# Kernel tuning notes

Measured on AMD Instinct MI355X. Metric: run time of the kernel, lower is better.

## Reference

```python
import jax, jax.numpy as jnp
import numpy as np

M, B, U, Z, H, X = 16, 2048, 16, 64, 512, 3072


def setup_inputs() -> dict:
    key = jax.random.key(0)
    ks = jax.random.split(key, 9)
    sc = lambda d: 1.0 / np.sqrt(d)
    return {
        "s": jax.random.normal(ks[0], (M, B, U + Z), dtype=jnp.float32),
        # per-mixture z2z: Linear(Z, Z); weights stored as [in, out]
        "Wzz": jax.random.normal(ks[1], (M, Z, Z), dtype=jnp.float32) * sc(Z),
        "bzz": jax.random.normal(ks[2], (M, Z), dtype=jnp.float32) * sc(Z),
        # per-mixture z2h: Linear(Z, H)
        "Wzh": jax.random.normal(ks[3], (M, Z, H), dtype=jnp.float32) * sc(Z),
        "bzh": jax.random.normal(ks[4], (M, H), dtype=jnp.float32) * sc(Z),
        # shared h2hd: Linear(H, H)
        "Whd": jax.random.normal(ks[5], (H, H), dtype=jnp.float32) * sc(H),
        "bhd": jax.random.normal(ks[6], (H,), dtype=jnp.float32) * sc(H),
        "Whx": jax.random.normal(ks[7], (H, X), dtype=jnp.float32) * sc(H),
        "bhx": jax.random.normal(ks[8], (X,), dtype=jnp.float32) * sc(H),
    }


def reference(s, Wzz, bzz, Wzh, bzh, Whd, bhd, Whx, bhx):
    # s: [M, B, U+Z]; split off z (u is unused in non-tvae mode)
    z = s[..., U:U + Z]                                   # [M, B, Z]
    # per-mixture z2z then z2h (batched over mixture dim), fused relu
    zz = jnp.einsum("mbz,mzy->mby", z, Wzz) + bzz[:, None, :]   # [M, B, Z]
    h = jax.nn.relu(jnp.einsum("mbz,mzh->mbh", zz, Wzh) + bzh[:, None, :])  # [M, B, H]
    # shared h2hd (num_layers == 1, h_dim_dec is None)
    h = jax.nn.relu(h @ Whd + bhd)                        # [M, B, H]
    xx = jax.nn.sigmoid(h @ Whx + bhx)                    # [M, B, X]
    return xx
```

## Files before the change

kernel.cpp:

```cpp
#include <hip/hip_runtime.h>
#include <stdint.h>

typedef __attribute__((ext_vector_type(4))) float f32x4;
typedef __attribute__((ext_vector_type(8))) short short8;

#define MM 16
#define BB 2048
#define UU 16
#define ZD 64
#define HH 512
#define XD 3072
#define RTOT (MM * BB)

#define MFMA16(a, b, c) __builtin_amdgcn_mfma_f32_16x16x32_bf16(a, b, c, 0, 0, 0)

static __device__ __forceinline__ unsigned short f2bf(float f) {
  union { float f; uint32_t u; } v; v.f = f;
  uint32_t r = v.u + 0x7fffu + ((v.u >> 16) & 1u);
  return (unsigned short)(r >> 16);
}

static __device__ __forceinline__ void async16(const void* g, void* l) {
  __builtin_amdgcn_global_load_lds(
      (const __attribute__((address_space(1))) uint32_t*)g,
      (__attribute__((address_space(3))) uint32_t*)l, 16, 0, 0);
}

static __device__ __forceinline__ void tr_tile(const float* __restrict__ in,
                                               unsigned short* __restrict__ out,
                                               int R, int C, int c0, int r0, int z,
                                               float (*tile)[33]) {
  const size_t base = (size_t)z * R * C;
  const int tx = threadIdx.x & 31, ty = threadIdx.x >> 5;
#pragma unroll
  for (int k = 0; k < 32; k += 8)
    tile[ty + k][tx] = in[base + (size_t)(r0 + ty + k) * C + c0 + tx];
  __syncthreads();
#pragma unroll
  for (int k = 0; k < 32; k += 8)
    out[base + (size_t)(c0 + ty + k) * R + r0 + tx] = f2bf(tile[tx][ty + k]);
}

__global__ __launch_bounds__(256) void trconv_all(
    const float* __restrict__ Wzz, const float* __restrict__ Wzh,
    const float* __restrict__ Whd, const float* __restrict__ Whx,
    unsigned short* __restrict__ wzzT, unsigned short* __restrict__ wzhT,
    unsigned short* __restrict__ whdT, unsigned short* __restrict__ whxT) {
  __shared__ float tile[32][33];
  int b = blockIdx.x;
  if (b < 64) {
    int l = b;
    tr_tile(Wzz, wzzT, 64, 64, (l & 1) * 32, ((l >> 1) & 1) * 32, l >> 2, tile);
  } else if (b < 576) {
    int l = b - 64;
    tr_tile(Wzh, wzhT, 64, 512, (l & 15) * 32, ((l >> 4) & 1) * 32, l >> 5, tile);
  } else if (b < 832) {
    int l = b - 576;
    tr_tile(Whd, whdT, 512, 512, (l & 15) * 32, (l >> 4) * 32, 0, tile);
  } else {
    int l = b - 832;
    tr_tile(Whx, whxT, 512, 3072, (l % 96) * 32, (l / 96) * 32, 0, tile);
  }
}

__global__ __launch_bounds__(256) void stage12(
    const float* __restrict__ s, const unsigned short* __restrict__ wzzT,
    const unsigned short* __restrict__ wzhT, const float* __restrict__ bzz,
    const float* __restrict__ bzh, unsigned short* __restrict__ h1) {
  __shared__ __align__(16) unsigned short zA[128 * 64];
  __shared__ __align__(16) unsigned short wzz[64 * 64];
  __shared__ __align__(16) unsigned short wbuf[2][128 * 64];
  const int m = blockIdx.y;
  const int m0r = blockIdx.x * 128;
  const int t = threadIdx.x, lane = t & 63, w = t >> 6;
  const int l15 = lane & 15, l4 = lane >> 4;

  {
    const unsigned short* g = wzzT + (size_t)m * 64 * 64;
    async16(g + t * 8, &wzz[t * 8]);
    async16(g + (t + 256) * 8, &wzz[(t + 256) * 8]);
    const unsigned short* gh = wzhT + (size_t)m * 512 * 64;
#pragma unroll
    for (int it = 0; it < 4; ++it) {
      int id = it * 256 + t;
      async16(gh + id * 8, &wbuf[0][id * 8]);
    }
  }
  const float* sb = s + ((size_t)m * BB + m0r) * (UU + ZD) + UU;
#pragma unroll
  for (int it = 0; it < 8; ++it) {
    int idx = it * 256 + t;
    int row = idx >> 4, f4 = idx & 15;
    const float4 v = *(const float4*)(sb + (size_t)row * (UU + ZD) + f4 * 4);
    ushort4 h;
    h.x = f2bf(v.x); h.y = f2bf(v.y); h.z = f2bf(v.z); h.w = f2bf(v.w);
    *(ushort4*)&zA[row * 64 + f4 * 4] = h;
  }
  __syncthreads();

  f32x4 acc1[2][4] = {};
#pragma unroll
  for (int ks = 0; ks < 2; ++ks) {
    short8 af[2], bf[4];
#pragma unroll
    for (int i = 0; i < 2; ++i)
      af[i] = *(const short8*)&zA[(w * 32 + i * 16 + l15) * 64 + ks * 32 + l4 * 8];
#pragma unroll
    for (int n = 0; n < 4; ++n)
      bf[n] = *(const short8*)&wzz[(n * 16 + l15) * 64 + ks * 32 + l4 * 8];
#pragma unroll
    for (int i = 0; i < 2; ++i)
#pragma unroll
      for (int n = 0; n < 4; ++n) acc1[i][n] = MFMA16(af[i], bf[n], acc1[i][n]);
  }
  {
    const unsigned short* gh = wzhT + (size_t)m * 512 * 64 + 128 * 64;
#pragma unroll
    for (int it = 0; it < 4; ++it) {
      int id = it * 256 + t;
      async16(gh + id * 8, &wbuf[1][id * 8]);
    }
  }
  __syncthreads();
  unsigned short* zzp = zA;
#pragma unroll
  for (int i = 0; i < 2; ++i)
#pragma unroll
    for (int n = 0; n < 4; ++n)
#pragma unroll
      for (int r = 0; r < 4; ++r) {
        int row = w * 32 + i * 16 + l4 * 4 + r;
        int col = n * 16 + l15;
        zzp[row * 64 + col] = f2bf(acc1[i][n][r] + bzz[m * 64 + col]);
      }
  __syncthreads();

  unsigned short* h1r = h1 + ((size_t)m * BB + m0r) * HH;
  for (int c = 0; c < 4; ++c) {
    f32x4 acc[2][8] = {};
#pragma unroll
    for (int ks = 0; ks < 2; ++ks) {
      short8 af[2], bf[8];
#pragma unroll
      for (int i = 0; i < 2; ++i)
        af[i] = *(const short8*)&zzp[(w * 32 + i * 16 + l15) * 64 + ks * 32 + l4 * 8];
#pragma unroll
      for (int n = 0; n < 8; ++n)
        bf[n] = *(const short8*)&wbuf[c & 1][(n * 16 + l15) * 64 + ks * 32 + l4 * 8];
#pragma unroll
      for (int i = 0; i < 2; ++i)
#pragma unroll
        for (int n = 0; n < 8; ++n) acc[i][n] = MFMA16(af[i], bf[n], acc[i][n]);
    }
#pragma unroll
    for (int i = 0; i < 2; ++i)
#pragma unroll
      for (int n = 0; n < 8; ++n)
#pragma unroll
        for (int r = 0; r < 4; ++r) {
          int row = w * 32 + i * 16 + l4 * 4 + r;
          int col = c * 128 + n * 16 + l15;
          float v = acc[i][n][r] + bzh[m * HH + col];
          h1r[(size_t)row * HH + col] = f2bf(fmaxf(v, 0.0f));
        }
    __syncthreads();
    if (c + 2 < 4) {
      const unsigned short* gh = wzhT + (size_t)m * 512 * 64 + (size_t)(c + 2) * 128 * 64;
#pragma unroll
      for (int it = 0; it < 4; ++it) {
        int id = it * 256 + t;
        async16(gh + id * 8, &wbuf[c & 1][id * 8]);
      }
    }
  }
}

template <int EPI, int Ntot, int Ktot>
__global__ __launch_bounds__(256) void gemm_bt(
    const unsigned short* __restrict__ A,
    const unsigned short* __restrict__ BT,
    const float* __restrict__ bias,
    void* __restrict__ outp) {
  __shared__ __align__(16) unsigned short lA[2][128 * 32];
  __shared__ __align__(16) unsigned short lB[2][128 * 32];
  const int t = threadIdx.x, lane = t & 63;
  const int wid = t >> 6, wr = wid >> 1, wc = wid & 1;
  const int l15 = lane & 15, l4 = lane >> 4;
  const int m0 = blockIdx.x * 128, n0 = blockIdx.y * 128;

  const int ra = t >> 2;
  const int sa = (t & 3) * 8;

  const unsigned short* gA = A + (size_t)m0 * Ktot;
  const unsigned short* gB = BT + (size_t)n0 * Ktot;

  float bv[4];
#pragma unroll
  for (int n = 0; n < 4; ++n) bv[n] = bias[n0 + wc * 64 + n * 16 + l15];

  f32x4 acc[4][4] = {};
  constexpr int NT = Ktot / 32;

  {
    const unsigned short* a0 = gA + (size_t)ra * Ktot + sa;
    const unsigned short* b0 = gB + (size_t)ra * Ktot + sa;
    async16(a0, &lA[0][t * 8]);
    async16(a0 + (size_t)64 * Ktot, &lA[0][(t + 256) * 8]);
    async16(b0, &lB[0][t * 8]);
    async16(b0 + (size_t)64 * Ktot, &lB[0][(t + 256) * 8]);
  }
  __syncthreads();
  for (int ks = 0; ks < NT; ++ks) {
    const int cur = ks & 1;
    if (ks + 1 < NT) {
      const int ko = (ks + 1) * 32;
      const unsigned short* a0 = gA + (size_t)ra * Ktot + ko + sa;
      const unsigned short* b0 = gB + (size_t)ra * Ktot + ko + sa;
      async16(a0, &lA[cur ^ 1][t * 8]);
      async16(a0 + (size_t)64 * Ktot, &lA[cur ^ 1][(t + 256) * 8]);
      async16(b0, &lB[cur ^ 1][t * 8]);
      async16(b0 + (size_t)64 * Ktot, &lB[cur ^ 1][(t + 256) * 8]);
    }
    short8 af[4], bf[4];
#pragma unroll
    for (int i = 0; i < 4; ++i)
      af[i] = *(const short8*)&lA[cur][(wr * 64 + i * 16 + l15) * 32 + l4 * 8];
#pragma unroll
    for (int n = 0; n < 4; ++n)
      bf[n] = *(const short8*)&lB[cur][(wc * 64 + n * 16 + l15) * 32 + l4 * 8];
#pragma unroll
    for (int i = 0; i < 4; ++i)
#pragma unroll
      for (int n = 0; n < 4; ++n) acc[i][n] = MFMA16(af[i], bf[n], acc[i][n]);
    __syncthreads();
  }

#pragma unroll
  for (int i = 0; i < 4; ++i)
#pragma unroll
    for (int n = 0; n < 4; ++n) {
      const int col = n0 + wc * 64 + n * 16 + l15;
#pragma unroll
      for (int r = 0; r < 4; ++r) {
        const int row = m0 + wr * 64 + i * 16 + l4 * 4 + r;
        float v = acc[i][n][r] + bv[n];
        if (EPI == 0) {
          ((unsigned short*)outp)[(size_t)row * Ntot + col] = f2bf(fmaxf(v, 0.0f));
        } else {
          v = 1.0f / (1.0f + __expf(-v));
          ((float*)outp)[(size_t)row * Ntot + col] = v;
        }
      }
    }
}

extern "C" void kernel_launch(void* const* d_in, const int* in_sizes, int n_in,
                              void* d_out, int out_size, void* d_ws, size_t ws_size,
                              hipStream_t stream) {
  const float* s   = (const float*)d_in[0];
  const float* Wzz = (const float*)d_in[1];
  const float* bzz = (const float*)d_in[2];
  const float* Wzh = (const float*)d_in[3];
  const float* bzh = (const float*)d_in[4];
  const float* Whd = (const float*)d_in[5];
  const float* bhd = (const float*)d_in[6];
  const float* Whx = (const float*)d_in[7];
  const float* bhx = (const float*)d_in[8];
  float* out = (float*)d_out;

  char* ws = (char*)d_ws;
  unsigned short* wzzT = (unsigned short*)ws; ws += (size_t)MM * 64 * 64 * 2;
  unsigned short* wzhT = (unsigned short*)ws; ws += (size_t)MM * 512 * 64 * 2;
  unsigned short* whdT = (unsigned short*)ws; ws += (size_t)512 * 512 * 2;
  unsigned short* whxT = (unsigned short*)ws; ws += (size_t)3072 * 512 * 2;
  unsigned short* h1   = (unsigned short*)ws; ws += (size_t)RTOT * 512 * 2;
  unsigned short* h2   = (unsigned short*)ws;

  dim3 blk(256);
  trconv_all<<<dim3(2368), blk, 0, stream>>>(Wzz, Wzh, Whd, Whx, wzzT, wzhT, whdT, whxT);
  stage12<<<dim3(16, 16), blk, 0, stream>>>(s, wzzT, wzhT, bzz, bzh, h1);
  gemm_bt<0, HH, HH><<<dim3(256, 4), blk, 0, stream>>>(h1, whdT, bhd, (void*)h2);
  gemm_bt<1, XD, HH><<<dim3(256, 24), blk, 0, stream>>>(h2, whxT, bhx, (void*)out);
}
```

Measured before the change: 592.0 us.

## Halve stage12 row tile and swizzle GEMM block order across XCDs

The stage12 kernel now handles 64 rows per block instead of 128, doubling its grid to 512 blocks for better CU occupancy on the small per-mixture stage. The two shared GEMMs switch to a 1D grid with a block-index swizzle that gives each of the 8 chiplets a contiguous range of tiles. The swizzle is meant to improve L2 reuse of A and B tiles. Smaller stage12 tiles mean each block reloads the Wzh weights for half the rows, adding weight traffic.

```diff
diff --git a/kernel.cpp b/kernel.cpp
--- a/kernel.cpp
+++ b/kernel.cpp
@@ -67,11 +67,11 @@
     const float* __restrict__ s, const unsigned short* __restrict__ wzzT,
     const unsigned short* __restrict__ wzhT, const float* __restrict__ bzz,
     const float* __restrict__ bzh, unsigned short* __restrict__ h1) {
-  __shared__ __align__(16) unsigned short zA[128 * 64];
+  __shared__ __align__(16) unsigned short zA[64 * 64];
   __shared__ __align__(16) unsigned short wzz[64 * 64];
   __shared__ __align__(16) unsigned short wbuf[2][128 * 64];
   const int m = blockIdx.y;
-  const int m0r = blockIdx.x * 128;
+  const int m0r = blockIdx.x * 64;
   const int t = threadIdx.x, lane = t & 63, w = t >> 6;
   const int l15 = lane & 15, l4 = lane >> 4;
 
@@ -88,7 +88,7 @@
   }
   const float* sb = s + ((size_t)m * BB + m0r) * (UU + ZD) + UU;
 #pragma unroll
-  for (int it = 0; it < 8; ++it) {
+  for (int it = 0; it < 4; ++it) {
     int idx = it * 256 + t;
     int row = idx >> 4, f4 = idx & 15;
     const float4 v = *(const float4*)(sb + (size_t)row * (UU + ZD) + f4 * 4);
@@ -98,20 +98,16 @@
   }
   __syncthreads();
 
-  f32x4 acc1[2][4] = {};
+  f32x4 acc1[4] = {};
 #pragma unroll
   for (int ks = 0; ks < 2; ++ks) {
-    short8 af[2], bf[4];
-#pragma unroll
-    for (int i = 0; i < 2; ++i)
-      af[i] = *(const short8*)&zA[(w * 32 + i * 16 + l15) * 64 + ks * 32 + l4 * 8];
+    short8 af, bf[4];
+    af = *(const short8*)&zA[(w * 16 + l15) * 64 + ks * 32 + l4 * 8];
 #pragma unroll
     for (int n = 0; n < 4; ++n)
       bf[n] = *(const short8*)&wzz[(n * 16 + l15) * 64 + ks * 32 + l4 * 8];
 #pragma unroll
-    for (int i = 0; i < 2; ++i)
-#pragma unroll
-      for (int n = 0; n < 4; ++n) acc1[i][n] = MFMA16(af[i], bf[n], acc1[i][n]);
+    for (int n = 0; n < 4; ++n) acc1[n] = MFMA16(af, bf[n], acc1[n]);
   }
   {
     const unsigned short* gh = wzhT + (size_t)m * 512 * 64 + 128 * 64;
@@ -124,45 +120,37 @@
   __syncthreads();
   unsigned short* zzp = zA;
 #pragma unroll
-  for (int i = 0; i < 2; ++i)
-#pragma unroll
-    for (int n = 0; n < 4; ++n)
-#pragma unroll
-      for (int r = 0; r < 4; ++r) {
-        int row = w * 32 + i * 16 + l4 * 4 + r;
-        int col = n * 16 + l15;
-        zzp[row * 64 + col] = f2bf(acc1[i][n][r] + bzz[m * 64 + col]);
-      }
+  for (int n = 0; n < 4; ++n)
+#pragma unroll
+    for (int r = 0; r < 4; ++r) {
+      int row = w * 16 + l4 * 4 + r;
+      int col = n * 16 + l15;
+      zzp[row * 64 + col] = f2bf(acc1[n][r] + bzz[m * 64 + col]);
+    }
   __syncthreads();
 
   unsigned short* h1r = h1 + ((size_t)m * BB + m0r) * HH;
   for (int c = 0; c < 4; ++c) {
-    f32x4 acc[2][8] = {};
+    f32x4 acc[8] = {};
 #pragma unroll
     for (int ks = 0; ks < 2; ++ks) {
-      short8 af[2], bf[8];
-#pragma unroll
-      for (int i = 0; i < 2; ++i)
-        af[i] = *(const short8*)&zzp[(w * 32 + i * 16 + l15) * 64 + ks * 32 + l4 * 8];
+      short8 af, bf[8];
+      af = *(const short8*)&zzp[(w * 16 + l15) * 64 + ks * 32 + l4 * 8];
 #pragma unroll
       for (int n = 0; n < 8; ++n)
         bf[n] = *(const short8*)&wbuf[c & 1][(n * 16 + l15) * 64 + ks * 32 + l4 * 8];
 #pragma unroll
-      for (int i = 0; i < 2; ++i)
-#pragma unroll
-        for (int n = 0; n < 8; ++n) acc[i][n] = MFMA16(af[i], bf[n], acc[i][n]);
-    }
-#pragma unroll
-    for (int i = 0; i < 2; ++i)
-#pragma unroll
-      for (int n = 0; n < 8; ++n)
-#pragma unroll
-        for (int r = 0; r < 4; ++r) {
-          int row = w * 32 + i * 16 + l4 * 4 + r;
-          int col = c * 128 + n * 16 + l15;
-          float v = acc[i][n][r] + bzh[m * HH + col];
-          h1r[(size_t)row * HH + col] = f2bf(fmaxf(v, 0.0f));
-        }
+      for (int n = 0; n < 8; ++n) acc[n] = MFMA16(af, bf[n], acc[n]);
+    }
+#pragma unroll
+    for (int n = 0; n < 8; ++n)
+#pragma unroll
+      for (int r = 0; r < 4; ++r) {
+        int row = w * 16 + l4 * 4 + r;
+        int col = c * 128 + n * 16 + l15;
+        float v = acc[n][r] + bzh[m * HH + col];
+        h1r[(size_t)row * HH + col] = f2bf(fmaxf(v, 0.0f));
+      }
     __syncthreads();
     if (c + 2 < 4) {
       const unsigned short* gh = wzhT + (size_t)m * 512 * 64 + (size_t)(c + 2) * 128 * 64;
@@ -175,7 +163,7 @@
   }
 }
 
-template <int EPI, int Ntot, int Ktot>
+template <int EPI, int Ntot, int Ktot, int MT, int NTL>
 __global__ __launch_bounds__(256) void gemm_bt(
     const unsigned short* __restrict__ A,
     const unsigned short* __restrict__ BT,
@@ -186,7 +174,13 @@
   const int t = threadIdx.x, lane = t & 63;
   const int wid = t >> 6, wr = wid >> 1, wc = wid & 1;
   const int l15 = lane & 15, l4 = lane >> 4;
-  const int m0 = blockIdx.x * 128, n0 = blockIdx.y * 128;
+
+  constexpr int nwg = MT * NTL;
+  constexpr int q = nwg / 8;
+  const int bid = blockIdx.x;
+  const int swz = (bid & 7) * q + (bid >> 3);
+  const int mt = swz / NTL, nt = swz % NTL;
+  const int m0 = mt * 128, n0 = nt * 128;
 
   const int ra = t >> 2;
   const int sa = (t & 3) * 8;
@@ -199,7 +193,7 @@
   for (int n = 0; n < 4; ++n) bv[n] = bias[n0 + wc * 64 + n * 16 + l15];
 
   f32x4 acc[4][4] = {};
-  constexpr int NT = Ktot / 32;
+  constexpr int KT = Ktot / 32;
 
   {
     const unsigned short* a0 = gA + (size_t)ra * Ktot + sa;
@@ -210,9 +204,9 @@
     async16(b0 + (size_t)64 * Ktot, &lB[0][(t + 256) * 8]);
   }
   __syncthreads();
-  for (int ks = 0; ks < NT; ++ks) {
+  for (int ks = 0; ks < KT; ++ks) {
     const int cur = ks & 1;
-    if (ks + 1 < NT) {
+    if (ks + 1 < KT) {
       const int ko = (ks + 1) * 32;
       const unsigned short* a0 = gA + (size_t)ra * Ktot + ko + sa;
       const unsigned short* b0 = gB + (size_t)ra * Ktot + ko + sa;
@@ -278,7 +272,7 @@
 
   dim3 blk(256);
   trconv_all<<<dim3(2368), blk, 0, stream>>>(Wzz, Wzh, Whd, Whx, wzzT, wzhT, whdT, whxT);
-  stage12<<<dim3(16, 16), blk, 0, stream>>>(s, wzzT, wzhT, bzz, bzh, h1);
-  gemm_bt<0, HH, HH><<<dim3(256, 4), blk, 0, stream>>>(h1, whdT, bhd, (void*)h2);
-  gemm_bt<1, XD, HH><<<dim3(256, 24), blk, 0, stream>>>(h2, whxT, bhx, (void*)out);
-}
+  stage12<<<dim3(32, 16), blk, 0, stream>>>(s, wzzT, wzhT, bzz, bzh, h1);
+  gemm_bt<0, HH, HH, 256, 4><<<dim3(1024), blk, 0, stream>>>(h1, whdT, bhd, (void*)h2);
+  gemm_bt<1, XD, HH, 256, 24><<<dim3(6144), blk, 0, stream>>>(h2, whxT, bhx, (void*)out);
+}
```

Result: faster. 569.4 us (-3.8%).
